# Performance work log

Measured on AMD Instinct MI355X. Metric: run time of the kernel, lower is better.

## Reference

```python
import jax, jax.numpy as jnp
import numpy as np

H = 16        # num_attention_heads
KVH = 4       # num_key_value_heads
D = 128       # head_dim
K = 5         # query multiplier k
HID = 2048    # hidden_size = H * D
THETA = 10000.0


def rotate_half(x):
    h = x.shape[-1] // 2
    return jnp.concatenate([-x[..., h:], x[..., :h]], axis=-1)


def setup_inputs() -> dict:
    key = jax.random.key(0)
    ks = jax.random.split(key, 6)
    B, S = 1, 1024
    q_len = S - 1
    hidden_states = jax.random.normal(ks[0], (B, S, HID), jnp.float32)
    prev_hidden_states = jax.random.normal(ks[1], (B, S - 1, HID), jnp.float32)
    causal = jnp.tril(jnp.ones((q_len, q_len), bool))
    attention_mask = jnp.where(causal, 0.0, -1e9).astype(jnp.float32)[None, None]  # (1,1,q,kv)
    position_ids = jnp.arange(q_len, dtype=jnp.int64)[None]  # (1, kv_len)
    Wq = jax.random.normal(ks[2], (HID, H * D * K), jnp.float32) * 0.02
    Wkv = jax.random.normal(ks[3], (2 * HID, 2 * KVH * D), jnp.float32) * 0.02
    Wo = jax.random.normal(ks[4], (HID, HID), jnp.float32) * 0.02
    return {
        'hidden_states': hidden_states,
        'prev_hidden_states': prev_hidden_states,
        'attention_mask': attention_mask,
        'position_ids': position_ids,
        'Wq': Wq,
        'Wkv': Wkv,
        'Wo': Wo,
    }


def reference(hidden_states, prev_hidden_states, attention_mask, position_ids, Wq, Wkv, Wo):
    B = hidden_states.shape[0]  # must be 1 for this module's broadcasting
    # feature-dim concat of previous layer states with shifted current states
    prev = jnp.concatenate([prev_hidden_states, hidden_states[:, :-1]], axis=-1)  # (B, S-1, 2*HID)
    hs = hidden_states[:, 1:]  # training-mode slice -> (B, q_len, HID)
    q_len = hs.shape[1]
    kv_len = prev.shape[1]

    q = hs @ Wq                       # (B, q_len, H*D*K)
    kv = prev @ Wkv                   # (B, kv_len, 2*KVH*D)
    k_st, v_st = jnp.split(kv, 2, axis=-1)

    # faithful raw reshape: (B, q_len, H*D*K) -> (B*K, q_len, H, D) -> (B*K, H, q_len, D)
    q = q.reshape(B * K, -1, H, D).transpose(0, 2, 1, 3)
    k_st = k_st.reshape(B, kv_len, KVH, D).transpose(0, 2, 1, 3)   # (B, KVH, kv, D)
    v_st = v_st.reshape(B, kv_len, KVH, D).transpose(0, 2, 1, 3)

    # RoPE (LlamaRotaryEmbedding)
    inv_freq = 1.0 / (THETA ** (jnp.arange(0, D, 2, dtype=jnp.float32) / D))  # (D/2,)
    freqs = position_ids.astype(jnp.float32)[..., None] * inv_freq            # (B, kv, D/2)
    emb = jnp.concatenate([freqs, freqs], axis=-1)                            # (B, kv, D)
    cos = jnp.cos(emb)[:, None]  # (B, 1, kv, D)
    sin = jnp.sin(emb)[:, None]
    q = q * cos[..., -q_len:, :] + rotate_half(q) * sin[..., -q_len:, :]
    k_st = k_st * cos[..., :kv_len, :] + rotate_half(k_st) * sin[..., :kv_len, :]

    # repeat_kv: (B, KVH, kv, D) -> (B, H, kv, D)
    n_rep = H // KVH
    k_rep = jnp.repeat(k_st, n_rep, axis=1)
    v_rep = jnp.repeat(v_st, n_rep, axis=1)

    # (B*K, H, q, D) @ (B, H, D, kv) -> broadcast over k variants (B==1)
    attn = jnp.matmul(q, jnp.swapaxes(k_rep, -1, -2)) / jnp.sqrt(jnp.float32(D))
    attn = attn + attention_mask
    attn = jax.nn.softmax(attn.astype(jnp.float32), axis=-1).astype(q.dtype)
    out = jnp.matmul(attn, v_rep)                 # (B*K, H, q, D)
    out = out.transpose(0, 2, 1, 3).reshape(B * K, q_len, HID)
    return out @ Wo                                # (B*K, q_len, HID)
```

## Files before the change

kernel.cpp:

```cpp
#include <hip/hip_runtime.h>
#include <cstddef>
#include <cstdint>

#define SQ    1023
#define HIDC  2048
#define NQC   10240
#define NKVC  1024

typedef unsigned short ushort_t;
typedef __bf16 bf16x8 __attribute__((ext_vector_type(8)));
typedef float  f32x4  __attribute__((ext_vector_type(4)));

__device__ __forceinline__ ushort_t f2bf(float x) {
  union { float f; uint32_t u; } v; v.f = x;
  uint32_t r = v.u + 0x7fffu + ((v.u >> 16) & 1u);
  return (ushort_t)(r >> 16);
}

__device__ __forceinline__ ushort_t f2bf_fast(float x) {
  __bf16 b = (__bf16)x;
  return __builtin_bit_cast(ushort_t, b);
}

__device__ __forceinline__ float fexp2(float x) {
  float r;
  asm("v_exp_f32 %0, %1\n\ts_nop 0" : "=v"(r) : "v"(x));
  return r;
}

__device__ __forceinline__ void fexp2x4(float& a, float& b, float& c, float& d) {
  asm("v_exp_f32 %0, %0\n\t"
      "v_exp_f32 %1, %1\n\t"
      "v_exp_f32 %2, %2\n\t"
      "v_exp_f32 %3, %3\n\t"
      "s_nop 0"
      : "+v"(a), "+v"(b), "+v"(c), "+v"(d));
}

__global__ void k_tables(float* __restrict__ cosT, float* __restrict__ sinT) {
  int idx = blockIdx.x * blockDim.x + threadIdx.x;
  if (idx >= SQ * 64) return;
  int t = idx >> 6, i = idx & 63;
  float inv = powf(10000.0f, -(float)i * (1.0f / 64.0f));
  float f = (float)t * inv;
  cosT[idx] = cosf(f);
  sinT[idx] = sinf(f);
}

__global__ void k_rope_k(const float* __restrict__ kvp, ushort_t* __restrict__ kb,
                         const float* __restrict__ cosT, const float* __restrict__ sinT) {
  int idx = blockIdx.x * blockDim.x + threadIdx.x;
  if (idx >= SQ * 4 * 64) return;
  int d   = idx & 63;
  int kvh = (idx >> 6) & 3;
  int t   = idx >> 8;
  size_t src = (size_t)t * 1024 + kvh * 128 + d;
  float x0 = 0.f, x1 = 0.f;
  #pragma unroll
  for (int z = 0; z < 4; ++z) {
    x0 += kvp[(size_t)z * (SQ * 1024) + src];
    x1 += kvp[(size_t)z * (SQ * 1024) + src + 64];
  }
  float c = cosT[t * 64 + d], s = sinT[t * 64 + d];
  size_t dst = (size_t)t * 512 + kvh * 128 + d;
  kb[dst]      = f2bf(x0 * c - x1 * s);
  kb[dst + 64] = f2bf(x1 * c + x0 * s);
}

__global__ __launch_bounds__(256)
void k_vtrans(const float* __restrict__ kvp, ushort_t* __restrict__ vt) {
  __shared__ float tile[32][33];
  int v0 = blockIdx.x * 32;
  int t0 = blockIdx.y * 32;
  int r = threadIdx.x >> 5, c = threadIdx.x & 31;
  #pragma unroll
  for (int p = 0; p < 4; ++p) {
    int t = t0 + p * 8 + r;
    float s = 0.f;
    if (t < SQ) {
      size_t src = (size_t)t * 1024 + 512 + v0 + c;
      #pragma unroll
      for (int z = 0; z < 4; ++z) s += kvp[(size_t)z * (SQ * 1024) + src];
    }
    tile[p * 8 + r][c] = s;
  }
  __syncthreads();
  #pragma unroll
  for (int p = 0; p < 4; ++p) {
    int v = v0 + p * 8 + r;
    vt[(size_t)v * 1024 + t0 + c] = f2bf(tile[c][p * 8 + r]);
  }
}

__global__ void k_prep(const float* __restrict__ hidden, const float* __restrict__ prevh,
                       ushort_t* __restrict__ hbf, ushort_t* __restrict__ akv) {
  int i = (blockIdx.x * blockDim.x + threadIdx.x) * 4;
  if (i >= SQ * 2048) return;
  int r = i >> 11, c = i & 2047;
  float4 h1 = *reinterpret_cast<const float4*>(hidden + (size_t)(r + 1) * 2048 + c);
  float4 h0 = *reinterpret_cast<const float4*>(hidden + (size_t)r * 2048 + c);
  float4 pv = *reinterpret_cast<const float4*>(prevh + (size_t)r * 2048 + c);
  uint2 a, b, d;
  a.x = (uint32_t)f2bf(h1.x) | ((uint32_t)f2bf(h1.y) << 16);
  a.y = (uint32_t)f2bf(h1.z) | ((uint32_t)f2bf(h1.w) << 16);
  b.x = (uint32_t)f2bf(pv.x) | ((uint32_t)f2bf(pv.y) << 16);
  b.y = (uint32_t)f2bf(pv.z) | ((uint32_t)f2bf(pv.w) << 16);
  d.x = (uint32_t)f2bf(h0.x) | ((uint32_t)f2bf(h0.y) << 16);
  d.y = (uint32_t)f2bf(h0.z) | ((uint32_t)f2bf(h0.w) << 16);
  *reinterpret_cast<uint2*>(hbf + i) = a;
  *reinterpret_cast<uint2*>(akv + (size_t)r * 4096 + c) = b;
  *reinterpret_cast<uint2*>(akv + (size_t)r * 4096 + 2048 + c) = d;
}

__global__ __launch_bounds__(256)
void k_tconv(const float* __restrict__ in, ushort_t* __restrict__ out, int K, int N) {
  __shared__ float t[32][33];
  int n0 = blockIdx.x * 32, k0 = blockIdx.y * 32;
  int r = threadIdx.x >> 5, c = threadIdx.x & 31;
  #pragma unroll
  for (int p = 0; p < 4; ++p)
    t[p * 8 + r][c] = in[(size_t)(k0 + p * 8 + r) * N + n0 + c];
  __syncthreads();
  #pragma unroll
  for (int p = 0; p < 4; ++p)
    out[(size_t)(n0 + p * 8 + r) * K + k0 + c] = f2bf(t[c][p * 8 + r]);
}

__global__ __launch_bounds__(256)
void k_gemm_rope(const ushort_t* __restrict__ A, const ushort_t* __restrict__ Bt,
                 ushort_t* __restrict__ Q, const float* __restrict__ cosT,
                 const float* __restrict__ sinT)
{
  const int Kd = 2048;
  __shared__ __align__(16) ushort_t As[3][128 * 32];
  __shared__ __align__(16) ushort_t Bs[3][128 * 32];

  const int tid  = threadIdx.x;
  const int lane = tid & 63;
  const int w    = tid >> 6;
  const int wm   = w >> 1, wn = w & 1;
  const int fr   = lane & 15;
  const int kg   = (lane >> 4) * 8;
  const int g4   = lane >> 4;
  const int m0   = blockIdx.y * 128, n0 = blockIdx.x * 128;

  const int lrow = lane >> 2;
  const int lk   = (lane & 3) * 8;

  f32x4 acc[4][4];
  #pragma unroll
  for (int i = 0; i < 4; ++i)
    #pragma unroll
    for (int j = 0; j < 4; ++j) acc[i][j] = (f32x4){0.f, 0.f, 0.f, 0.f};

  auto STAGE = [&](int b, int k0) {
    #pragma unroll
    for (int c = 0; c < 2; ++c) {
      int ch  = w + c * 4;
      int row = ch * 16 + lrow;
      const ushort_t* ga = A  + (size_t)(m0 + row) * Kd + k0 + lk;
      const ushort_t* gb = Bt + (size_t)(n0 + row) * Kd + k0 + lk;
      __builtin_amdgcn_global_load_lds(
          (const __attribute__((address_space(1))) void*)ga,
          (__attribute__((address_space(3))) void*)(&As[b][0] + ch * 512), 16, 0, 0);
      __builtin_amdgcn_global_load_lds(
          (const __attribute__((address_space(1))) void*)gb,
          (__attribute__((address_space(3))) void*)(&Bs[b][0] + ch * 512), 16, 0, 0);
    }
  };

  const int nt = Kd / 32;
  STAGE(0, 0);
  STAGE(1, 32);

  int cur = 0;
  for (int t = 0; t < nt; ++t) {
    if (t + 1 < nt) {
      asm volatile("s_waitcnt vmcnt(4)" ::: "memory");
    } else {
      asm volatile("s_waitcnt vmcnt(0)" ::: "memory");
    }
    __builtin_amdgcn_s_barrier();
    if (t + 2 < nt) {
      int sb = cur + 2; if (sb >= 3) sb -= 3;
      STAGE(sb, (t + 2) * 32);
    }

    bf16x8 av[4], bv[4];
    #pragma unroll
    for (int mi = 0; mi < 4; ++mi)
      av[mi] = *reinterpret_cast<const bf16x8*>(&As[cur][0] + (wm * 64 + mi * 16 + fr) * 32 + kg);
    #pragma unroll
    for (int nj = 0; nj < 4; ++nj) {
      int colOff = wn * 32 + (nj & 1) * 16 + (nj >> 1) * 64;
      bv[nj] = *reinterpret_cast<const bf16x8*>(&Bs[cur][0] + (colOff + fr) * 32 + kg);
    }
    #pragma unroll
    for (int mi = 0; mi < 4; ++mi)
      #pragma unroll
      for (int nj = 0; nj < 4; ++nj)
        acc[mi][nj] = __builtin_amdgcn_mfma_f32_16x16x32_bf16(av[mi], bv[nj], acc[mi][nj], 0, 0, 0);

    cur = (cur == 2) ? 0 : cur + 1;
  }

  const float sc = 0.1275174485f;
  const int nChunk = n0 >> 11;
  #pragma unroll
  for (int mi = 0; mi < 4; ++mi) {
    #pragma unroll
    for (int r = 0; r < 4; ++r) {
      int gr = m0 + wm * 64 + mi * 16 + g4 * 4 + r;
      if (gr >= SQ) continue;
      int st  = gr * 5 + nChunk;
      int tau = st % 1023;
      const float* ct = cosT + tau * 64;
      const float* stb = sinT + tau * 64;
      #pragma unroll
      for (int njp = 0; njp < 2; ++njp) {
        int dd = wn * 32 + njp * 16 + fr;
        float c = ct[dd], s = stb[dd];
        float x0 = acc[mi][njp][r];
        float x1 = acc[mi][njp + 2][r];
        size_t base = (size_t)gr * 10240 + n0 + dd;
        Q[base]      = f2bf_fast((x0 * c - x1 * s) * sc);
        Q[base + 64] = f2bf_fast((x1 * c + x0 * s) * sc);
      }
    }
  }
}

__global__ __launch_bounds__(256)
void k_gemm3buf(const ushort_t* __restrict__ A, const ushort_t* __restrict__ Bt,
                float* __restrict__ C, int M, int N, int Kd)
{
  __shared__ __align__(16) ushort_t As[3][128 * 32];
  __shared__ __align__(16) ushort_t Bs[3][128 * 32];

  const int tid  = threadIdx.x;
  const int lane = tid & 63;
  const int w    = tid >> 6;
  const int wm   = w >> 1, wn = w & 1;
  const int fr   = lane & 15;
  const int kg   = (lane >> 4) * 8;
  const int m0   = blockIdx.y * 128, n0 = blockIdx.x * 128;

  const int lrow = lane >> 2;
  const int lk   = (lane & 3) * 8;

  f32x4 acc[4][4];
  #pragma unroll
  for (int i = 0; i < 4; ++i)
    #pragma unroll
    for (int j = 0; j < 4; ++j) acc[i][j] = (f32x4){0.f, 0.f, 0.f, 0.f};

  auto STAGE = [&](int b, int k0) {
    #pragma unroll
    for (int c = 0; c < 2; ++c) {
      int ch  = w + c * 4;
      int row = ch * 16 + lrow;
      const ushort_t* ga = A  + (size_t)(m0 + row) * Kd + k0 + lk;
      const ushort_t* gb = Bt + (size_t)(n0 + row) * Kd + k0 + lk;
      __builtin_amdgcn_global_load_lds(
          (const __attribute__((address_space(1))) void*)ga,
          (__attribute__((address_space(3))) void*)(&As[b][0] + ch * 512), 16, 0, 0);
      __builtin_amdgcn_global_load_lds(
          (const __attribute__((address_space(1))) void*)gb,
          (__attribute__((address_space(3))) void*)(&Bs[b][0] + ch * 512), 16, 0, 0);
    }
  };

  const int nt = Kd / 32;
  STAGE(0, 0);
  STAGE(1, 32);

  int cur = 0;
  for (int t = 0; t < nt; ++t) {
    if (t + 1 < nt) {
      asm volatile("s_waitcnt vmcnt(4)" ::: "memory");
    } else {
      asm volatile("s_waitcnt vmcnt(0)" ::: "memory");
    }
    __builtin_amdgcn_s_barrier();
    if (t + 2 < nt) {
      int sb = cur + 2; if (sb >= 3) sb -= 3;
      STAGE(sb, (t + 2) * 32);
    }

    bf16x8 av[4], bv[4];
    #pragma unroll
    for (int mi = 0; mi < 4; ++mi)
      av[mi] = *reinterpret_cast<const bf16x8*>(&As[cur][0] + (wm * 64 + mi * 16 + fr) * 32 + kg);
    #pragma unroll
    for (int nj = 0; nj < 4; ++nj)
      bv[nj] = *reinterpret_cast<const bf16x8*>(&Bs[cur][0] + (wn * 64 + nj * 16 + fr) * 32 + kg);
    #pragma unroll
    for (int mi = 0; mi < 4; ++mi)
      #pragma unroll
      for (int nj = 0; nj < 4; ++nj)
        acc[mi][nj] = __builtin_amdgcn_mfma_f32_16x16x32_bf16(av[mi], bv[nj], acc[mi][nj], 0, 0, 0);

    cur = (cur == 2) ? 0 : cur + 1;
  }

  #pragma unroll
  for (int mi = 0; mi < 4; ++mi) {
    #pragma unroll
    for (int nj = 0; nj < 4; ++nj) {
      int rbase = m0 + wm * 64 + mi * 16 + (lane >> 4) * 4;
      int col   = n0 + wn * 64 + nj * 16 + fr;
      #pragma unroll
      for (int r = 0; r < 4; ++r) {
        int gr = rbase + r;
        if (gr < M) C[(size_t)gr * N + col] = acc[mi][nj][r];
      }
    }
  }
}

__global__ __launch_bounds__(256)
void k_gemm64(const ushort_t* __restrict__ A, const ushort_t* __restrict__ Bt,
              float* __restrict__ C, int M, int N, int Kd, int kLen)
{
  __shared__ __align__(16) ushort_t As[64 * 32];
  __shared__ __align__(16) ushort_t Bs[128 * 32];

  const int tid  = threadIdx.x;
  const int lane = tid & 63;
  const int w    = tid >> 6;
  const int wm   = w >> 1, wn = w & 1;
  const int fr   = lane & 15;
  const int kg   = (lane >> 4) * 8;
  const int g4   = lane >> 4;
  const int l15  = lane & 15;
  const int m0   = blockIdx.y * 64, n0 = blockIdx.x * 128;
  const int kOff = blockIdx.z * kLen;
  C += (size_t)blockIdx.z * M * N;

  const int arow = tid >> 2, aslot = (tid & 3) * 8;

  f32x4 acc[2][4];
  #pragma unroll
  for (int i = 0; i < 2; ++i)
    #pragma unroll
    for (int j = 0; j < 4; ++j) acc[i][j] = (f32x4){0.f, 0.f, 0.f, 0.f};

  for (int k0 = kOff; k0 < kOff + kLen; k0 += 32) {
    {
      const ushort_t* ga = A + (size_t)(m0 + arow) * Kd + k0 + aslot;
      __builtin_amdgcn_global_load_lds(
          (const __attribute__((address_space(1))) void*)ga,
          (__attribute__((address_space(3))) void*)(As + w * 512), 16, 0, 0);
    }
    #pragma unroll
    for (int c = 0; c < 2; ++c) {
      int u = c * 256 + tid;
      const ushort_t* gb = Bt + (size_t)(n0 + (u >> 2)) * Kd + k0 + (u & 3) * 8;
      __builtin_amdgcn_global_load_lds(
          (const __attribute__((address_space(1))) void*)gb,
          (__attribute__((address_space(3))) void*)(Bs + (c * 256 + w * 64) * 8), 16, 0, 0);
    }
    __syncthreads();

    bf16x8 av[2], bv[4];
    #pragma unroll
    for (int mi = 0; mi < 2; ++mi)
      av[mi] = *reinterpret_cast<const bf16x8*>(As + (wm * 32 + mi * 16 + fr) * 32 + kg);
    #pragma unroll
    for (int nj = 0; nj < 4; ++nj)
      bv[nj] = *reinterpret_cast<const bf16x8*>(Bs + (wn * 64 + nj * 16 + fr) * 32 + kg);
    #pragma unroll
    for (int mi = 0; mi < 2; ++mi)
      #pragma unroll
      for (int nj = 0; nj < 4; ++nj)
        acc[mi][nj] = __builtin_amdgcn_mfma_f32_16x16x32_bf16(av[mi], bv[nj], acc[mi][nj], 0, 0, 0);
    __syncthreads();
  }

  #pragma unroll
  for (int mi = 0; mi < 2; ++mi) {
    #pragma unroll
    for (int nj = 0; nj < 4; ++nj) {
      int rbase = m0 + wm * 32 + mi * 16 + g4 * 4;
      int col   = n0 + wn * 64 + nj * 16 + l15;
      #pragma unroll
      for (int r = 0; r < 4; ++r) {
        int gr = rbase + r;
        if (gr < M) C[(size_t)gr * N + col] = acc[mi][nj][r];
      }
    }
  }
}

__global__ __launch_bounds__(256)
void k_attn_mfma(const ushort_t* __restrict__ qb, const ushort_t* __restrict__ kb,
                 const ushort_t* __restrict__ vt, ushort_t* __restrict__ oattb)
{
  __shared__ __align__(16) ushort_t Ks[64 * 128];
  __shared__ __align__(16) ushort_t Vs[128 * 64];
  __shared__ __align__(16) ushort_t Ps[4][16 * 64];

  const int tid  = threadIdx.x;
  const int lane = tid & 63;
  const int w    = tid >> 6;
  const int l15  = lane & 15;
  const int g4   = lane >> 4;
  const int gh   = blockIdx.x;
  const int g = gh >> 4, h = gh & 15, kvh = (gh & 15) >> 2;
  const int qt = 15 - blockIdx.y;
  const int t0 = qt * 64;

  bf16x8 av[4];
  {
    int t = t0 + w * 16 + l15;
    const ushort_t* qrow = qb + (((size_t)(g * SQ + t)) * 16 + h) * 128;
    #pragma unroll
    for (int kk = 0; kk < 4; ++kk)
      av[kk] = *reinterpret_cast<const bf16x8*>(qrow + kk * 32 + g4 * 8);
  }

  bf16x8 ones;
  #pragma unroll
  for (int j = 0; j < 8; ++j) ones[j] = __builtin_bit_cast(__bf16, (ushort_t)0x3F80);

  f32x4 acc[8];
  #pragma unroll
  for (int dt = 0; dt < 8; ++dt) acc[dt] = (f32x4){0.f, 0.f, 0.f, 0.f};
  f32x4 acc_l = (f32x4){0.f, 0.f, 0.f, 0.f};
  float m[4];
  #pragma unroll
  for (int r = 0; r < 4; ++r) m[r] = -1e30f;

  ushort_t* pw = &Ps[w][0];

  for (int jt = 0; jt <= qt; ++jt) {
    int u0 = jt * 64;
    #pragma unroll
    for (int i = 0; i < 4; ++i) {
      int c = (w * 4 + i) * 64 + lane;
      int kv = c >> 4, sl = c & 15;
      const ushort_t* srck = kb + (size_t)(u0 + kv) * 512 + kvh * 128 + ((sl ^ (kv & 7)) << 3);
      __builtin_amdgcn_global_load_lds(
          (const __attribute__((address_space(1))) void*)srck,
          (__attribute__((address_space(3))) void*)(Ks + (w * 4 + i) * 512), 16, 0, 0);
      int d = c >> 3, sv = c & 7;
      const ushort_t* srcv = vt + (size_t)(kvh * 128 + d) * 1024 + u0 + ((sv ^ (d & 7)) << 3);
      __builtin_amdgcn_global_load_lds(
          (const __attribute__((address_space(1))) void*)srcv,
          (__attribute__((address_space(3))) void*)(Vs + (w * 4 + i) * 512), 16, 0, 0);
    }
    __syncthreads();

    f32x4 S[4];
    #pragma unroll
    for (int ct = 0; ct < 4; ++ct) S[ct] = (f32x4){0.f, 0.f, 0.f, 0.f};
    #pragma unroll
    for (int ct = 0; ct < 4; ++ct) {
      int kv = ct * 16 + l15;
      #pragma unroll
      for (int kk = 0; kk < 4; ++kk) {
        bf16x8 bv = *reinterpret_cast<const bf16x8*>(
            Ks + kv * 128 + ((((kk << 2) | g4) ^ (kv & 7)) << 3));
        S[ct] = __builtin_amdgcn_mfma_f32_16x16x32_bf16(av[kk], bv, S[ct], 0, 0, 0);
      }
    }
    if (jt == qt) {
      #pragma unroll
      for (int ct = 0; ct < 4; ++ct) {
        int u = u0 + ct * 16 + l15;
        #pragma unroll
        for (int r = 0; r < 4; ++r) {
          int t = t0 + w * 16 + g4 * 4 + r;
          if (u > t) S[ct][r] = -1e30f;
        }
      }
    }
    float tm[4];
    #pragma unroll
    for (int r = 0; r < 4; ++r) {
      float t1 = fmaxf(fmaxf(S[0][r], S[1][r]), fmaxf(S[2][r], S[3][r]));
      t1 = fmaxf(t1, __shfl_xor(t1, 1));
      t1 = fmaxf(t1, __shfl_xor(t1, 2));
      t1 = fmaxf(t1, __shfl_xor(t1, 4));
      t1 = fmaxf(t1, __shfl_xor(t1, 8));
      tm[r] = t1;
    }
    bool need = (tm[0] > m[0] + 8.f) || (tm[1] > m[1] + 8.f) ||
                (tm[2] > m[2] + 8.f) || (tm[3] > m[3] + 8.f);
    if (__any(need)) {
      #pragma unroll
      for (int r = 0; r < 4; ++r) {
        float mn = fmaxf(m[r], tm[r]);
        float corr = fexp2(m[r] - mn);
        m[r] = mn;
        acc_l[r] *= corr;
        #pragma unroll
        for (int dt = 0; dt < 8; ++dt) acc[dt][r] *= corr;
      }
    }
    #pragma unroll
    for (int r = 0; r < 4; ++r) {
      float e0 = S[0][r] - m[r];
      float e1 = S[1][r] - m[r];
      float e2 = S[2][r] - m[r];
      float e3 = S[3][r] - m[r];
      fexp2x4(e0, e1, e2, e3);
      S[0][r] = e0; S[1][r] = e1; S[2][r] = e2; S[3][r] = e3;
    }

    #pragma unroll
    for (int ct = 0; ct < 4; ++ct) {
      int kv = ct * 16 + l15;
      #pragma unroll
      for (int r = 0; r < 4; ++r) {
        int q = g4 * 4 + r;
        pw[q * 64 + ((((kv >> 3) ^ (q & 7)) << 3) | (kv & 7))] = f2bf_fast(S[ct][r]);
      }
    }
    #pragma unroll
    for (int kk = 0; kk < 2; ++kk) {
      bf16x8 pa = *reinterpret_cast<const bf16x8*>(
          pw + l15 * 64 + ((((kk << 2) | g4) ^ (l15 & 7)) << 3));
      acc_l = __builtin_amdgcn_mfma_f32_16x16x32_bf16(pa, ones, acc_l, 0, 0, 0);
      #pragma unroll
      for (int dt = 0; dt < 8; ++dt) {
        int d = dt * 16 + l15;
        bf16x8 vv = *reinterpret_cast<const bf16x8*>(
            Vs + d * 64 + ((((kk << 2) | g4) ^ (d & 7)) << 3));
        acc[dt] = __builtin_amdgcn_mfma_f32_16x16x32_bf16(pa, vv, acc[dt], 0, 0, 0);
      }
    }
    __syncthreads();
  }

  #pragma unroll
  for (int r = 0; r < 4; ++r) {
    int t = t0 + w * 16 + g4 * 4 + r;
    if (t >= SQ) continue;
    float inv = 1.f / acc_l[r];
    ushort_t* dst = oattb + ((size_t)(g * SQ + t)) * 2048 + h * 128;
    #pragma unroll
    for (int dt = 0; dt < 8; ++dt)
      dst[dt * 16 + l15] = f2bf_fast(acc[dt][r] * inv);
  }
}

extern "C" void kernel_launch(void* const* d_in, const int* in_sizes, int n_in,
                              void* d_out, int out_size, void* d_ws, size_t ws_size,
                              hipStream_t stream) {
  const float* hidden = (const float*)d_in[0];
  const float* prevh  = (const float*)d_in[1];
  const float* Wq     = (const float*)d_in[4];
  const float* Wkv    = (const float*)d_in[5];
  const float* Wo     = (const float*)d_in[6];
  float* out = (float*)d_out;

  char* ws = (char*)d_ws;
  float*    kvp   = (float*)ws;                        ws += (size_t)4 * SQ * 1024 * 4;
  float*    cosT  = (float*)ws;                        ws += (size_t)65472 * 4;
  float*    sinT  = (float*)ws;                        ws += (size_t)65472 * 4;
  ushort_t* qbb   = (ushort_t*)ws;                     ws += (size_t)5120 * 2048 * 2;
  ushort_t* kb    = (ushort_t*)ws;                     ws += (size_t)1024 * 512 * 2;
  ushort_t* vtb   = (ushort_t*)ws;                     ws += (size_t)512 * 1024 * 2;
  ushort_t* hbf   = (ushort_t*)ws;                     ws += (size_t)1024 * 2048 * 2;
  ushort_t* akv   = (ushort_t*)ws;                     ws += (size_t)1024 * 4096 * 2;
  ushort_t* oattb = (ushort_t*)ws;                     ws += (size_t)5120 * 2048 * 2;
  ushort_t* wqt   = (ushort_t*)ws;                     ws += (size_t)10240 * 2048 * 2;
  ushort_t* wkvt  = (ushort_t*)ws;                     ws += (size_t)1024 * 4096 * 2;
  ushort_t* wot   = (ushort_t*)ws;                     ws += (size_t)2048 * 2048 * 2;

  k_tables<<<dim3((SQ * 64 + 255) / 256), dim3(256), 0, stream>>>(cosT, sinT);

  k_tconv<<<dim3(NQC / 32, HIDC / 32), dim3(256), 0, stream>>>(Wq, wqt, HIDC, NQC);
  k_tconv<<<dim3(NKVC / 32, 4096 / 32), dim3(256), 0, stream>>>(Wkv, wkvt, 4096, NKVC);
  k_tconv<<<dim3(HIDC / 32, HIDC / 32), dim3(256), 0, stream>>>(Wo, wot, HIDC, HIDC);

  k_prep<<<dim3((SQ * 2048 / 4 + 255) / 256), dim3(256), 0, stream>>>(hidden, prevh, hbf, akv);

  k_gemm_rope<<<dim3(NQC / 128, 8), dim3(256), 0, stream>>>(hbf, wqt, qbb, cosT, sinT);
  k_gemm64<<<dim3(NKVC / 128, 16, 4), dim3(256), 0, stream>>>(akv, wkvt, kvp, SQ, NKVC, 4096, 1024);

  k_rope_k<<<dim3((SQ * 4 * 64 + 255) / 256), dim3(256), 0, stream>>>(kvp, kb, cosT, sinT);
  k_vtrans<<<dim3(16, 32), dim3(256), 0, stream>>>(kvp, vtb);

  k_attn_mfma<<<dim3(80, 16), dim3(256), 0, stream>>>(qbb, kb, vtb, oattb);

  k_gemm3buf<<<dim3(HIDC / 128, 40), dim3(256), 0, stream>>>(oattb, wot, out, 5115, HIDC, 2048);
}
```

Before: 269.7 us.

## Merge independent preprocessing, GEMM, and KV kernels into combined launches

Combines the table, weight-transpose, and input-conversion kernels into one launch that picks its role from the block index. The Q projection GEMM and the split-K KV GEMM now share one launch, and the K-RoPE and V-transpose kernels share another. The aim is to cut launch overhead and the idle tail between small dependent kernels so that independent work overlaps on the GPU. In exchange, a merged kernel uses the larger LDS and register footprint of its heaviest branch for every block, which can lower occupancy.

```diff
diff --git a/kernel.cpp b/kernel.cpp
--- a/kernel.cpp
+++ b/kernel.cpp
@@ -37,86 +37,12 @@
       : "+v"(a), "+v"(b), "+v"(c), "+v"(d));
 }
 
-__global__ void k_tables(float* __restrict__ cosT, float* __restrict__ sinT) {
-  int idx = blockIdx.x * blockDim.x + threadIdx.x;
-  if (idx >= SQ * 64) return;
-  int t = idx >> 6, i = idx & 63;
-  float inv = powf(10000.0f, -(float)i * (1.0f / 64.0f));
-  float f = (float)t * inv;
-  cosT[idx] = cosf(f);
-  sinT[idx] = sinf(f);
-}
-
-__global__ void k_rope_k(const float* __restrict__ kvp, ushort_t* __restrict__ kb,
-                         const float* __restrict__ cosT, const float* __restrict__ sinT) {
-  int idx = blockIdx.x * blockDim.x + threadIdx.x;
-  if (idx >= SQ * 4 * 64) return;
-  int d   = idx & 63;
-  int kvh = (idx >> 6) & 3;
-  int t   = idx >> 8;
-  size_t src = (size_t)t * 1024 + kvh * 128 + d;
-  float x0 = 0.f, x1 = 0.f;
-  #pragma unroll
-  for (int z = 0; z < 4; ++z) {
-    x0 += kvp[(size_t)z * (SQ * 1024) + src];
-    x1 += kvp[(size_t)z * (SQ * 1024) + src + 64];
-  }
-  float c = cosT[t * 64 + d], s = sinT[t * 64 + d];
-  size_t dst = (size_t)t * 512 + kvh * 128 + d;
-  kb[dst]      = f2bf(x0 * c - x1 * s);
-  kb[dst + 64] = f2bf(x1 * c + x0 * s);
-}
-
-__global__ __launch_bounds__(256)
-void k_vtrans(const float* __restrict__ kvp, ushort_t* __restrict__ vt) {
-  __shared__ float tile[32][33];
-  int v0 = blockIdx.x * 32;
-  int t0 = blockIdx.y * 32;
-  int r = threadIdx.x >> 5, c = threadIdx.x & 31;
-  #pragma unroll
-  for (int p = 0; p < 4; ++p) {
-    int t = t0 + p * 8 + r;
-    float s = 0.f;
-    if (t < SQ) {
-      size_t src = (size_t)t * 1024 + 512 + v0 + c;
-      #pragma unroll
-      for (int z = 0; z < 4; ++z) s += kvp[(size_t)z * (SQ * 1024) + src];
-    }
-    tile[p * 8 + r][c] = s;
-  }
-  __syncthreads();
-  #pragma unroll
-  for (int p = 0; p < 4; ++p) {
-    int v = v0 + p * 8 + r;
-    vt[(size_t)v * 1024 + t0 + c] = f2bf(tile[c][p * 8 + r]);
-  }
-}
-
-__global__ void k_prep(const float* __restrict__ hidden, const float* __restrict__ prevh,
-                       ushort_t* __restrict__ hbf, ushort_t* __restrict__ akv) {
-  int i = (blockIdx.x * blockDim.x + threadIdx.x) * 4;
-  if (i >= SQ * 2048) return;
-  int r = i >> 11, c = i & 2047;
-  float4 h1 = *reinterpret_cast<const float4*>(hidden + (size_t)(r + 1) * 2048 + c);
-  float4 h0 = *reinterpret_cast<const float4*>(hidden + (size_t)r * 2048 + c);
-  float4 pv = *reinterpret_cast<const float4*>(prevh + (size_t)r * 2048 + c);
-  uint2 a, b, d;
-  a.x = (uint32_t)f2bf(h1.x) | ((uint32_t)f2bf(h1.y) << 16);
-  a.y = (uint32_t)f2bf(h1.z) | ((uint32_t)f2bf(h1.w) << 16);
-  b.x = (uint32_t)f2bf(pv.x) | ((uint32_t)f2bf(pv.y) << 16);
-  b.y = (uint32_t)f2bf(pv.z) | ((uint32_t)f2bf(pv.w) << 16);
-  d.x = (uint32_t)f2bf(h0.x) | ((uint32_t)f2bf(h0.y) << 16);
-  d.y = (uint32_t)f2bf(h0.z) | ((uint32_t)f2bf(h0.w) << 16);
-  *reinterpret_cast<uint2*>(hbf + i) = a;
-  *reinterpret_cast<uint2*>(akv + (size_t)r * 4096 + c) = b;
-  *reinterpret_cast<uint2*>(akv + (size_t)r * 4096 + 2048 + c) = d;
-}
-
-__global__ __launch_bounds__(256)
-void k_tconv(const float* __restrict__ in, ushort_t* __restrict__ out, int K, int N) {
-  __shared__ float t[32][33];
-  int n0 = blockIdx.x * 32, k0 = blockIdx.y * 32;
-  int r = threadIdx.x >> 5, c = threadIdx.x & 31;
+__device__ __forceinline__ void tconv_body(const float* __restrict__ in,
+                                           ushort_t* __restrict__ out,
+                                           int K, int N, int bx, int by,
+                                           int tid, float (&t)[32][33]) {
+  int n0 = bx * 32, k0 = by * 32;
+  int r = tid >> 5, c = tid & 31;
   #pragma unroll
   for (int p = 0; p < 4; ++p)
     t[p * 8 + r][c] = in[(size_t)(k0 + p * 8 + r) * N + n0 + c];
@@ -127,11 +53,61 @@
 }
 
 __global__ __launch_bounds__(256)
-void k_gemm_rope(const ushort_t* __restrict__ A, const ushort_t* __restrict__ Bt,
-                 ushort_t* __restrict__ Q, const float* __restrict__ cosT,
-                 const float* __restrict__ sinT)
+void k_pre(const float* __restrict__ Wq, const float* __restrict__ Wkv,
+           const float* __restrict__ Wo, const float* __restrict__ hidden,
+           const float* __restrict__ prevh,
+           ushort_t* __restrict__ wqt, ushort_t* __restrict__ wkvt,
+           ushort_t* __restrict__ wot, ushort_t* __restrict__ hbf,
+           ushort_t* __restrict__ akv,
+           float* __restrict__ cosT, float* __restrict__ sinT)
 {
-  const int Kd = 2048;
+  __shared__ float tsh[32][33];
+  const int tid = threadIdx.x;
+  int b = blockIdx.x;
+  if (b < 20480) { tconv_body(Wq, wqt, HIDC, NQC, b % 320, b / 320, tid, tsh); return; }
+  b -= 20480;
+  if (b < 4096)  { tconv_body(Wkv, wkvt, 4096, NKVC, b % 32, b / 32, tid, tsh); return; }
+  b -= 4096;
+  if (b < 4096)  { tconv_body(Wo, wot, HIDC, HIDC, b % 64, b / 64, tid, tsh); return; }
+  b -= 4096;
+  if (b < 2046) {
+    int i = (b * 256 + tid) * 4;
+    if (i >= SQ * 2048) return;
+    int r = i >> 11, c = i & 2047;
+    float4 h1 = *reinterpret_cast<const float4*>(hidden + (size_t)(r + 1) * 2048 + c);
+    float4 h0 = *reinterpret_cast<const float4*>(hidden + (size_t)r * 2048 + c);
+    float4 pv = *reinterpret_cast<const float4*>(prevh + (size_t)r * 2048 + c);
+    uint2 a, bb, d;
+    a.x  = (uint32_t)f2bf(h1.x) | ((uint32_t)f2bf(h1.y) << 16);
+    a.y  = (uint32_t)f2bf(h1.z) | ((uint32_t)f2bf(h1.w) << 16);
+    bb.x = (uint32_t)f2bf(pv.x) | ((uint32_t)f2bf(pv.y) << 16);
+    bb.y = (uint32_t)f2bf(pv.z) | ((uint32_t)f2bf(pv.w) << 16);
+    d.x  = (uint32_t)f2bf(h0.x) | ((uint32_t)f2bf(h0.y) << 16);
+    d.y  = (uint32_t)f2bf(h0.z) | ((uint32_t)f2bf(h0.w) << 16);
+    *reinterpret_cast<uint2*>(hbf + i) = a;
+    *reinterpret_cast<uint2*>(akv + (size_t)r * 4096 + c) = bb;
+    *reinterpret_cast<uint2*>(akv + (size_t)r * 4096 + 2048 + c) = d;
+    return;
+  }
+  b -= 2046;
+  {
+    int idx = b * 256 + tid;
+    if (idx >= SQ * 64) return;
+    int t = idx >> 6, i = idx & 63;
+    float inv = powf(10000.0f, -(float)i * (1.0f / 64.0f));
+    float f = (float)t * inv;
+    cosT[idx] = cosf(f);
+    sinT[idx] = sinf(f);
+  }
+}
+
+__global__ __launch_bounds__(256)
+void k_gemms(const ushort_t* __restrict__ hbf, const ushort_t* __restrict__ wqt,
+             ushort_t* __restrict__ qbb, const float* __restrict__ cosT,
+             const float* __restrict__ sinT,
+             const ushort_t* __restrict__ akv, const ushort_t* __restrict__ wkvt,
+             float* __restrict__ kvp)
+{
   __shared__ __align__(16) ushort_t As[3][128 * 32];
   __shared__ __align__(16) ushort_t Bs[3][128 * 32];
 
@@ -142,6 +118,227 @@
   const int fr   = lane & 15;
   const int kg   = (lane >> 4) * 8;
   const int g4   = lane >> 4;
+  const int lrow = lane >> 2;
+  const int lk   = (lane & 3) * 8;
+
+  if (blockIdx.x < 640) {
+    const int Kd = 2048;
+    const int m0 = (blockIdx.x / 80) * 128, n0 = (blockIdx.x % 80) * 128;
+    const ushort_t* A  = hbf;
+    const ushort_t* Bt = wqt;
+
+    f32x4 acc[4][4];
+    #pragma unroll
+    for (int i = 0; i < 4; ++i)
+      #pragma unroll
+      for (int j = 0; j < 4; ++j) acc[i][j] = (f32x4){0.f, 0.f, 0.f, 0.f};
+
+    auto STAGE = [&](int b, int k0) {
+      #pragma unroll
+      for (int c = 0; c < 2; ++c) {
+        int ch  = w + c * 4;
+        int row = ch * 16 + lrow;
+        const ushort_t* ga = A  + (size_t)(m0 + row) * Kd + k0 + lk;
+        const ushort_t* gb = Bt + (size_t)(n0 + row) * Kd + k0 + lk;
+        __builtin_amdgcn_global_load_lds(
+            (const __attribute__((address_space(1))) void*)ga,
+            (__attribute__((address_space(3))) void*)(&As[b][0] + ch * 512), 16, 0, 0);
+        __builtin_amdgcn_global_load_lds(
+            (const __attribute__((address_space(1))) void*)gb,
+            (__attribute__((address_space(3))) void*)(&Bs[b][0] + ch * 512), 16, 0, 0);
+      }
+    };
+
+    const int nt = Kd / 32;
+    STAGE(0, 0);
+    STAGE(1, 32);
+
+    int cur = 0;
+    for (int t = 0; t < nt; ++t) {
+      if (t + 1 < nt) {
+        asm volatile("s_waitcnt vmcnt(4)" ::: "memory");
+      } else {
+        asm volatile("s_waitcnt vmcnt(0)" ::: "memory");
+      }
+      __builtin_amdgcn_s_barrier();
+      if (t + 2 < nt) {
+        int sb = cur + 2; if (sb >= 3) sb -= 3;
+        STAGE(sb, (t + 2) * 32);
+      }
+
+      bf16x8 av[4], bv[4];
+      #pragma unroll
+      for (int mi = 0; mi < 4; ++mi)
+        av[mi] = *reinterpret_cast<const bf16x8*>(&As[cur][0] + (wm * 64 + mi * 16 + fr) * 32 + kg);
+      #pragma unroll
+      for (int nj = 0; nj < 4; ++nj) {
+        int colOff = wn * 32 + (nj & 1) * 16 + (nj >> 1) * 64;
+        bv[nj] = *reinterpret_cast<const bf16x8*>(&Bs[cur][0] + (colOff + fr) * 32 + kg);
+      }
+      #pragma unroll
+      for (int mi = 0; mi < 4; ++mi)
+        #pragma unroll
+        for (int nj = 0; nj < 4; ++nj)
+          acc[mi][nj] = __builtin_amdgcn_mfma_f32_16x16x32_bf16(av[mi], bv[nj], acc[mi][nj], 0, 0, 0);
+
+      cur = (cur == 2) ? 0 : cur + 1;
+    }
+
+    const float sc = 0.1275174485f;
+    const int nChunk = n0 >> 11;
+    #pragma unroll
+    for (int mi = 0; mi < 4; ++mi) {
+      #pragma unroll
+      for (int r = 0; r < 4; ++r) {
+        int gr = m0 + wm * 64 + mi * 16 + g4 * 4 + r;
+        if (gr >= SQ) continue;
+        int st  = gr * 5 + nChunk;
+        int tau = st % 1023;
+        const float* ct  = cosT + tau * 64;
+        const float* stb = sinT + tau * 64;
+        #pragma unroll
+        for (int njp = 0; njp < 2; ++njp) {
+          int dd = wn * 32 + njp * 16 + fr;
+          float c = ct[dd], s = stb[dd];
+          float x0 = acc[mi][njp][r];
+          float x1 = acc[mi][njp + 2][r];
+          size_t base = (size_t)gr * 10240 + n0 + dd;
+          qbb[base]      = f2bf_fast((x0 * c - x1 * s) * sc);
+          qbb[base + 64] = f2bf_fast((x1 * c + x0 * s) * sc);
+        }
+      }
+    }
+  } else {
+    const int u = blockIdx.x - 640;
+    const int Kd = 4096, M = SQ, N = NKVC, kLen = 1024;
+    const int n0 = (u & 7) * 128, m0 = ((u >> 3) & 15) * 64;
+    const int kOff = (u >> 7) * kLen;
+    float* C = kvp + (size_t)(u >> 7) * M * N;
+    ushort_t* As64 = &As[0][0];
+    ushort_t* Bs64 = &Bs[0][0];
+
+    const int arow = tid >> 2, aslot = (tid & 3) * 8;
+    const int l15 = lane & 15;
+
+    f32x4 acc[2][4];
+    #pragma unroll
+    for (int i = 0; i < 2; ++i)
+      #pragma unroll
+      for (int j = 0; j < 4; ++j) acc[i][j] = (f32x4){0.f, 0.f, 0.f, 0.f};
+
+    for (int k0 = kOff; k0 < kOff + kLen; k0 += 32) {
+      {
+        const ushort_t* ga = akv + (size_t)(m0 + arow) * Kd + k0 + aslot;
+        __builtin_amdgcn_global_load_lds(
+            (const __attribute__((address_space(1))) void*)ga,
+            (__attribute__((address_space(3))) void*)(As64 + w * 512), 16, 0, 0);
+      }
+      #pragma unroll
+      for (int c = 0; c < 2; ++c) {
+        int uu = c * 256 + tid;
+        const ushort_t* gb = wkvt + (size_t)(n0 + (uu >> 2)) * Kd + k0 + (uu & 3) * 8;
+        __builtin_amdgcn_global_load_lds(
+            (const __attribute__((address_space(1))) void*)gb,
+            (__attribute__((address_space(3))) void*)(Bs64 + (c * 256 + w * 64) * 8), 16, 0, 0);
+      }
+      __syncthreads();
+
+      bf16x8 av[2], bv[4];
+      #pragma unroll
+      for (int mi = 0; mi < 2; ++mi)
+        av[mi] = *reinterpret_cast<const bf16x8*>(As64 + (wm * 32 + mi * 16 + fr) * 32 + kg);
+      #pragma unroll
+      for (int nj = 0; nj < 4; ++nj)
+        bv[nj] = *reinterpret_cast<const bf16x8*>(Bs64 + (wn * 64 + nj * 16 + fr) * 32 + kg);
+      #pragma unroll
+      for (int mi = 0; mi < 2; ++mi)
+        #pragma unroll
+        for (int nj = 0; nj < 4; ++nj)
+          acc[mi][nj] = __builtin_amdgcn_mfma_f32_16x16x32_bf16(av[mi], bv[nj], acc[mi][nj], 0, 0, 0);
+      __syncthreads();
+    }
+
+    #pragma unroll
+    for (int mi = 0; mi < 2; ++mi) {
+      #pragma unroll
+      for (int nj = 0; nj < 4; ++nj) {
+        int rbase = m0 + wm * 32 + mi * 16 + g4 * 4;
+        int col   = n0 + wn * 64 + nj * 16 + l15;
+        #pragma unroll
+        for (int r = 0; r < 4; ++r) {
+          int gr = rbase + r;
+          if (gr < M) C[(size_t)gr * N + col] = acc[mi][nj][r];
+        }
+      }
+    }
+  }
+}
+
+__global__ __launch_bounds__(256)
+void k_kv(const float* __restrict__ kvp, ushort_t* __restrict__ kb,
+          ushort_t* __restrict__ vt, const float* __restrict__ cosT,
+          const float* __restrict__ sinT)
+{
+  __shared__ float tile[32][33];
+  const int tid = threadIdx.x;
+  int b = blockIdx.x;
+  if (b < 1023) {
+    int idx = b * 256 + tid;
+    if (idx >= SQ * 4 * 64) return;
+    int d   = idx & 63;
+    int kvh = (idx >> 6) & 3;
+    int t   = idx >> 8;
+    size_t src = (size_t)t * 1024 + kvh * 128 + d;
+    float x0 = 0.f, x1 = 0.f;
+    #pragma unroll
+    for (int z = 0; z < 4; ++z) {
+      x0 += kvp[(size_t)z * (SQ * 1024) + src];
+      x1 += kvp[(size_t)z * (SQ * 1024) + src + 64];
+    }
+    float c = cosT[t * 64 + d], s = sinT[t * 64 + d];
+    size_t dst = (size_t)t * 512 + kvh * 128 + d;
+    kb[dst]      = f2bf(x0 * c - x1 * s);
+    kb[dst + 64] = f2bf(x1 * c + x0 * s);
+    return;
+  }
+  b -= 1023;
+  {
+    int v0 = (b & 15) * 32;
+    int t0 = (b >> 4) * 32;
+    int r = tid >> 5, c = tid & 31;
+    #pragma unroll
+    for (int p = 0; p < 4; ++p) {
+      int t = t0 + p * 8 + r;
+      float s = 0.f;
+      if (t < SQ) {
+        size_t src = (size_t)t * 1024 + 512 + v0 + c;
+        #pragma unroll
+        for (int z = 0; z < 4; ++z) s += kvp[(size_t)z * (SQ * 1024) + src];
+      }
+      tile[p * 8 + r][c] = s;
+    }
+    __syncthreads();
+    #pragma unroll
+    for (int p = 0; p < 4; ++p) {
+      int v = v0 + p * 8 + r;
+      vt[(size_t)v * 1024 + t0 + c] = f2bf(tile[c][p * 8 + r]);
+    }
+  }
+}
+
+__global__ __launch_bounds__(256)
+void k_gemm3buf(const ushort_t* __restrict__ A, const ushort_t* __restrict__ Bt,
+                float* __restrict__ C, int M, int N, int Kd)
+{
+  __shared__ __align__(16) ushort_t As[3][128 * 32];
+  __shared__ __align__(16) ushort_t Bs[3][128 * 32];
+
+  const int tid  = threadIdx.x;
+  const int lane = tid & 63;
+  const int w    = tid >> 6;
+  const int wm   = w >> 1, wn = w & 1;
+  const int fr   = lane & 15;
+  const int kg   = (lane >> 4) * 8;
   const int m0   = blockIdx.y * 128, n0 = blockIdx.x * 128;
 
   const int lrow = lane >> 2;
@@ -191,107 +388,6 @@
     for (int mi = 0; mi < 4; ++mi)
       av[mi] = *reinterpret_cast<const bf16x8*>(&As[cur][0] + (wm * 64 + mi * 16 + fr) * 32 + kg);
     #pragma unroll
-    for (int nj = 0; nj < 4; ++nj) {
-      int colOff = wn * 32 + (nj & 1) * 16 + (nj >> 1) * 64;
-      bv[nj] = *reinterpret_cast<const bf16x8*>(&Bs[cur][0] + (colOff + fr) * 32 + kg);
-    }
-    #pragma unroll
-    for (int mi = 0; mi < 4; ++mi)
-      #pragma unroll
-      for (int nj = 0; nj < 4; ++nj)
-        acc[mi][nj] = __builtin_amdgcn_mfma_f32_16x16x32_bf16(av[mi], bv[nj], acc[mi][nj], 0, 0, 0);
-
-    cur = (cur == 2) ? 0 : cur + 1;
-  }
-
-  const float sc = 0.1275174485f;
-  const int nChunk = n0 >> 11;
-  #pragma unroll
-  for (int mi = 0; mi < 4; ++mi) {
-    #pragma unroll
-    for (int r = 0; r < 4; ++r) {
-      int gr = m0 + wm * 64 + mi * 16 + g4 * 4 + r;
-      if (gr >= SQ) continue;
-      int st  = gr * 5 + nChunk;
-      int tau = st % 1023;
-      const float* ct = cosT + tau * 64;
-      const float* stb = sinT + tau * 64;
-      #pragma unroll
-      for (int njp = 0; njp < 2; ++njp) {
-        int dd = wn * 32 + njp * 16 + fr;
-        float c = ct[dd], s = stb[dd];
-        float x0 = acc[mi][njp][r];
-        float x1 = acc[mi][njp + 2][r];
-        size_t base = (size_t)gr * 10240 + n0 + dd;
-        Q[base]      = f2bf_fast((x0 * c - x1 * s) * sc);
-        Q[base + 64] = f2bf_fast((x1 * c + x0 * s) * sc);
-      }
-    }
-  }
-}
-
-__global__ __launch_bounds__(256)
-void k_gemm3buf(const ushort_t* __restrict__ A, const ushort_t* __restrict__ Bt,
-                float* __restrict__ C, int M, int N, int Kd)
-{
-  __shared__ __align__(16) ushort_t As[3][128 * 32];
-  __shared__ __align__(16) ushort_t Bs[3][128 * 32];
-
-  const int tid  = threadIdx.x;
-  const int lane = tid & 63;
-  const int w    = tid >> 6;
-  const int wm   = w >> 1, wn = w & 1;
-  const int fr   = lane & 15;
-  const int kg   = (lane >> 4) * 8;
-  const int m0   = blockIdx.y * 128, n0 = blockIdx.x * 128;
-
-  const int lrow = lane >> 2;
-  const int lk   = (lane & 3) * 8;
-
-  f32x4 acc[4][4];
-  #pragma unroll
-  for (int i = 0; i < 4; ++i)
-    #pragma unroll
-    for (int j = 0; j < 4; ++j) acc[i][j] = (f32x4){0.f, 0.f, 0.f, 0.f};
-
-  auto STAGE = [&](int b, int k0) {
-    #pragma unroll
-    for (int c = 0; c < 2; ++c) {
-      int ch  = w + c * 4;
-      int row = ch * 16 + lrow;
-      const ushort_t* ga = A  + (size_t)(m0 + row) * Kd + k0 + lk;
-      const ushort_t* gb = Bt + (size_t)(n0 + row) * Kd + k0 + lk;
-      __builtin_amdgcn_global_load_lds(
-          (const __attribute__((address_space(1))) void*)ga,
-          (__attribute__((address_space(3))) void*)(&As[b][0] + ch * 512), 16, 0, 0);
-      __builtin_amdgcn_global_load_lds(
-          (const __attribute__((address_space(1))) void*)gb,
-          (__attribute__((address_space(3))) void*)(&Bs[b][0] + ch * 512), 16, 0, 0);
-    }
-  };
-
-  const int nt = Kd / 32;
-  STAGE(0, 0);
-  STAGE(1, 32);
-
-  int cur = 0;
-  for (int t = 0; t < nt; ++t) {
-    if (t + 1 < nt) {
-      asm volatile("s_waitcnt vmcnt(4)" ::: "memory");
-    } else {
-      asm volatile("s_waitcnt vmcnt(0)" ::: "memory");
-    }
-    __builtin_amdgcn_s_barrier();
-    if (t + 2 < nt) {
-      int sb = cur + 2; if (sb >= 3) sb -= 3;
-      STAGE(sb, (t + 2) * 32);
-    }
-
-    bf16x8 av[4], bv[4];
-    #pragma unroll
-    for (int mi = 0; mi < 4; ++mi)
-      av[mi] = *reinterpret_cast<const bf16x8*>(&As[cur][0] + (wm * 64 + mi * 16 + fr) * 32 + kg);
-    #pragma unroll
     for (int nj = 0; nj < 4; ++nj)
       bv[nj] = *reinterpret_cast<const bf16x8*>(&Bs[cur][0] + (wn * 64 + nj * 16 + fr) * 32 + kg);
     #pragma unroll
@@ -309,80 +405,6 @@
     for (int nj = 0; nj < 4; ++nj) {
       int rbase = m0 + wm * 64 + mi * 16 + (lane >> 4) * 4;
       int col   = n0 + wn * 64 + nj * 16 + fr;
-      #pragma unroll
-      for (int r = 0; r < 4; ++r) {
-        int gr = rbase + r;
-        if (gr < M) C[(size_t)gr * N + col] = acc[mi][nj][r];
-      }
-    }
-  }
-}
-
-__global__ __launch_bounds__(256)
-void k_gemm64(const ushort_t* __restrict__ A, const ushort_t* __restrict__ Bt,
-              float* __restrict__ C, int M, int N, int Kd, int kLen)
-{
-  __shared__ __align__(16) ushort_t As[64 * 32];
-  __shared__ __align__(16) ushort_t Bs[128 * 32];
-
-  const int tid  = threadIdx.x;
-  const int lane = tid & 63;
-  const int w    = tid >> 6;
-  const int wm   = w >> 1, wn = w & 1;
-  const int fr   = lane & 15;
-  const int kg   = (lane >> 4) * 8;
-  const int g4   = lane >> 4;
-  const int l15  = lane & 15;
-  const int m0   = blockIdx.y * 64, n0 = blockIdx.x * 128;
-  const int kOff = blockIdx.z * kLen;
-  C += (size_t)blockIdx.z * M * N;
-
-  const int arow = tid >> 2, aslot = (tid & 3) * 8;
-
-  f32x4 acc[2][4];
-  #pragma unroll
-  for (int i = 0; i < 2; ++i)
-    #pragma unroll
-    for (int j = 0; j < 4; ++j) acc[i][j] = (f32x4){0.f, 0.f, 0.f, 0.f};
-
-  for (int k0 = kOff; k0 < kOff + kLen; k0 += 32) {
-    {
-      const ushort_t* ga = A + (size_t)(m0 + arow) * Kd + k0 + aslot;
-      __builtin_amdgcn_global_load_lds(
-          (const __attribute__((address_space(1))) void*)ga,
-          (__attribute__((address_space(3))) void*)(As + w * 512), 16, 0, 0);
-    }
-    #pragma unroll
-    for (int c = 0; c < 2; ++c) {
-      int u = c * 256 + tid;
-      const ushort_t* gb = Bt + (size_t)(n0 + (u >> 2)) * Kd + k0 + (u & 3) * 8;
-      __builtin_amdgcn_global_load_lds(
-          (const __attribute__((address_space(1))) void*)gb,
-          (__attribute__((address_space(3))) void*)(Bs + (c * 256 + w * 64) * 8), 16, 0, 0);
-    }
-    __syncthreads();
-
-    bf16x8 av[2], bv[4];
-    #pragma unroll
-    for (int mi = 0; mi < 2; ++mi)
-      av[mi] = *reinterpret_cast<const bf16x8*>(As + (wm * 32 + mi * 16 + fr) * 32 + kg);
-    #pragma unroll
-    for (int nj = 0; nj < 4; ++nj)
-      bv[nj] = *reinterpret_cast<const bf16x8*>(Bs + (wn * 64 + nj * 16 + fr) * 32 + kg);
-    #pragma unroll
-    for (int mi = 0; mi < 2; ++mi)
-      #pragma unroll
-      for (int nj = 0; nj < 4; ++nj)
-        acc[mi][nj] = __builtin_amdgcn_mfma_f32_16x16x32_bf16(av[mi], bv[nj], acc[mi][nj], 0, 0, 0);
-    __syncthreads();
-  }
-
-  #pragma unroll
-  for (int mi = 0; mi < 2; ++mi) {
-    #pragma unroll
-    for (int nj = 0; nj < 4; ++nj) {
-      int rbase = m0 + wm * 32 + mi * 16 + g4 * 4;
-      int col   = n0 + wn * 64 + nj * 16 + l15;
       #pragma unroll
       for (int r = 0; r < 4; ++r) {
         int gr = rbase + r;
@@ -569,19 +591,13 @@
   ushort_t* wkvt  = (ushort_t*)ws;                     ws += (size_t)1024 * 4096 * 2;
   ushort_t* wot   = (ushort_t*)ws;                     ws += (size_t)2048 * 2048 * 2;
 
-  k_tables<<<dim3((SQ * 64 + 255) / 256), dim3(256), 0, stream>>>(cosT, sinT);
-
-  k_tconv<<<dim3(NQC / 32, HIDC / 32), dim3(256), 0, stream>>>(Wq, wqt, HIDC, NQC);
-  k_tconv<<<dim3(NKVC / 32, 4096 / 32), dim3(256), 0, stream>>>(Wkv, wkvt, 4096, NKVC);
-  k_tconv<<<dim3(HIDC / 32, HIDC / 32), dim3(256), 0, stream>>>(Wo, wot, HIDC, HIDC);
-
-  k_prep<<<dim3((SQ * 2048 / 4 + 255) / 256), dim3(256), 0, stream>>>(hidden, prevh, hbf, akv);
-
-  k_gemm_rope<<<dim3(NQC / 128, 8), dim3(256), 0, stream>>>(hbf, wqt, qbb, cosT, sinT);
-  k_gemm64<<<dim3(NKVC / 128, 16, 4), dim3(256), 0, stream>>>(akv, wkvt, kvp, SQ, NKVC, 4096, 1024);
-
-  k_rope_k<<<dim3((SQ * 4 * 64 + 255) / 256), dim3(256), 0, stream>>>(kvp, kb, cosT, sinT);
-  k_vtrans<<<dim3(16, 32), dim3(256), 0, stream>>>(kvp, vtb);
+  k_pre<<<dim3(20480 + 4096 + 4096 + 2046 + 256), dim3(256), 0, stream>>>(
+      Wq, Wkv, Wo, hidden, prevh, wqt, wkvt, wot, hbf, akv, cosT, sinT);
+
+  k_gemms<<<dim3(1152), dim3(256), 0, stream>>>(
+      hbf, wqt, qbb, cosT, sinT, akv, wkvt, kvp);
+
+  k_kv<<<dim3(1023 + 512), dim3(256), 0, stream>>>(kvp, kb, vtb, cosT, sinT);
 
   k_attn_mfma<<<dim3(80, 16), dim3(256), 0, stream>>>(qbb, kb, vtb, oattb);
 
```

New measurement: 245.6 us. -8.9%, faster.
